# Kernel tuning notes

Hardware: AMD Instinct MI355X
Metric: run time of the kernel (lower is better)

Reference implementation:

```python
import jax, jax.numpy as jnp
import numpy as np

N_NODES = 100000
N_EDGES = 1600000
IN_F = 128
HID_F = 128
N_CLS = 40


def _linear_params(key, out_f, in_f):
    k1, k2 = jax.random.split(key)
    s = 1.0 / np.sqrt(in_f)
    w = jax.random.uniform(k1, (out_f, in_f), jnp.float32, -s, s)
    b = jax.random.uniform(k2, (out_f,), jnp.float32, -s, s)
    return w, b


def setup_inputs() -> dict:
    key = jax.random.key(0)
    ks = jax.random.split(key, 9)
    in_feat = jax.random.normal(ks[0], (N_NODES, IN_F), jnp.float32)
    src = jax.random.randint(ks[1], (N_EDGES,), 0, N_NODES, jnp.int32)
    dst = jax.random.randint(ks[2], (N_EDGES,), 0, N_NODES, jnp.int32)
    pool_w1, pool_b1 = _linear_params(ks[3], IN_F, IN_F)
    self_w1, self_b1 = _linear_params(ks[4], HID_F, IN_F)
    neigh_w1, neigh_b1 = _linear_params(ks[5], HID_F, IN_F)
    pool_w2, pool_b2 = _linear_params(ks[6], HID_F, HID_F)
    self_w2, self_b2 = _linear_params(ks[7], N_CLS, HID_F)
    neigh_w2, neigh_b2 = _linear_params(ks[8], N_CLS, HID_F)
    return dict(in_feat=in_feat, src=src, dst=dst,
                pool_w1=pool_w1, pool_b1=pool_b1, self_w1=self_w1, self_b1=self_b1,
                neigh_w1=neigh_w1, neigh_b1=neigh_b1,
                pool_w2=pool_w2, pool_b2=pool_b2, self_w2=self_w2, self_b2=self_b2,
                neigh_w2=neigh_w2, neigh_b2=neigh_b2)


def sage_conv_pool(h, src, dst, pool_w, pool_b, self_w, self_b, neigh_w, neigh_b):
    # fc_pool + relu on nodes first (N < E), then gather per edge
    m = jax.nn.relu(h @ pool_w.T + pool_b)            # [N, d]
    msgs = m[src]                                     # [E, d] gather
    agg = jax.ops.segment_max(msgs, dst, num_segments=N_NODES)  # [N, d]
    agg = jnp.where(jnp.isfinite(agg), agg, 0.0)      # zero for isolated nodes
    return h @ self_w.T + self_b + agg @ neigh_w.T + neigh_b


def reference(in_feat, src, dst,
              pool_w1, pool_b1, self_w1, self_b1, neigh_w1, neigh_b1,
              pool_w2, pool_b2, self_w2, self_b2, neigh_w2, neigh_b2):
    h = sage_conv_pool(in_feat, src, dst, pool_w1, pool_b1, self_w1, self_b1, neigh_w1, neigh_b1)
    h = jax.nn.relu(h)  # dropout is identity in eval mode
    h = sage_conv_pool(h, src, dst, pool_w2, pool_b2, self_w2, self_b2, neigh_w2, neigh_b2)
    return h
```

## Files before the change

kernel.cpp:

```cpp
#include <hip/hip_runtime.h>


#define N_FEAT 128
#define NWG_A 256
#define BSHIFT 10
#define NBMAX 128

typedef __attribute__((ext_vector_type(8))) short bf16x8;
typedef __attribute__((ext_vector_type(8))) unsigned short u16x8;
typedef __attribute__((ext_vector_type(4))) float f32x4;

static __device__ __forceinline__ unsigned short f2bf(float f) {
    unsigned u = __float_as_uint(f);
    unsigned r = (u + 0x7fffu + ((u >> 16) & 1u)) >> 16;
    return (unsigned short)r;
}

static __device__ __forceinline__ bf16x8 loadA_f32(const float* __restrict__ A, size_t idx) {
    float4 a = *(const float4*)&A[idx];
    float4 b = *(const float4*)&A[idx + 4];
    bf16x8 r;
    r[0] = (short)f2bf(a.x); r[1] = (short)f2bf(a.y);
    r[2] = (short)f2bf(a.z); r[3] = (short)f2bf(a.w);
    r[4] = (short)f2bf(b.x); r[5] = (short)f2bf(b.y);
    r[6] = (short)f2bf(b.z); r[7] = (short)f2bf(b.w);
    return r;
}

__global__ __launch_bounds__(256) void prep_bin_kernel(
    const float* __restrict__ pw1, const float* __restrict__ sw1,
    const float* __restrict__ nw1, const float* __restrict__ pw2,
    const float* __restrict__ sw2, const float* __restrict__ nw2,
    const float* __restrict__ sb1, const float* __restrict__ nb1,
    const float* __restrict__ sb2, const float* __restrict__ nb2,
    unsigned short* __restrict__ wb_p1, unsigned short* __restrict__ wb_s1,
    unsigned short* __restrict__ wb_n1, unsigned short* __restrict__ wb_p2,
    unsigned short* __restrict__ wb_s2, unsigned short* __restrict__ wb_n2,
    float* __restrict__ b_sn1, float* __restrict__ b_sn2,
    const int* __restrict__ dst, int* __restrict__ wgcnt, int E, int NB)
{
    __shared__ int cnt[NBMAX];
    if (blockIdx.x < NWG_A) {
        const int wg = blockIdx.x, tid = threadIdx.x;
        if (tid < NB) cnt[tid] = 0;
        __syncthreads();
        const int slab = (E + NWG_A - 1) / NWG_A;
        const int e0 = wg * slab;
        const int e1 = min(e0 + slab, E);
        for (int e = e0 + tid; e < e1; e += 256)
            atomicAdd(&cnt[dst[e] >> BSHIFT], 1);
        __syncthreads();
        if (tid < NB) wgcnt[tid * NWG_A + wg] = cnt[tid];
    } else {
        int t = (blockIdx.x - NWG_A) * 256 + threadIdx.x;
        if (t < 16384) {
            wb_p1[t] = f2bf(pw1[t]);
            wb_s1[t] = f2bf(sw1[t]);
            wb_n1[t] = f2bf(nw1[t]);
            wb_p2[t] = f2bf(pw2[t]);
        }
        if (t < 6144) {
            int row = t >> 7;
            wb_s2[t] = (row < 40) ? f2bf(sw2[t]) : 0;
            wb_n2[t] = (row < 40) ? f2bf(nw2[t]) : 0;
        }
        if (t < 128) b_sn1[t] = sb1[t] + nb1[t];
        if (t < 64)  b_sn2[t] = (t < 40) ? (sb2[t] + nb2[t]) : 0.f;
    }
}

__global__ __launch_bounds__(1024) void bin_scan_kernel(const int* __restrict__ wgcnt,
                                                        int* __restrict__ binoff, int NB)
{
    __shared__ int sh[1024];
    const int t = threadIdx.x;
    const int total = NB * NWG_A;
    const int chunk = (total + 1023) / 1024;
    const int b0 = t * chunk;
    const int b1 = min(b0 + chunk, total);
    int s = 0;
    for (int k = b0; k < b1; k++) s += wgcnt[k];
    sh[t] = s;
    __syncthreads();
    for (int off = 1; off < 1024; off <<= 1) {
        int x = (t >= off) ? sh[t - off] : 0;
        __syncthreads();
        sh[t] += x;
        __syncthreads();
    }
    int run = sh[t] - s;
    for (int k = b0; k < b1; k++) {
        int v = wgcnt[k];
        binoff[k] = run;
        run += v;
    }
    if (t == 1023) binoff[total] = sh[1023];
}

__global__ __launch_bounds__(256, 4) void scatter_pool_kernel(
    const int* __restrict__ src, const int* __restrict__ dst,
    const int* __restrict__ binoff, unsigned* __restrict__ binned, int E, int NB,
    const float* __restrict__ A0f, const unsigned short* __restrict__ B0,
    const float* __restrict__ bias, unsigned short* __restrict__ Cout, int M)
{
    __shared__ int cur[NBMAX];
    __shared__ unsigned short Bs[128 * 136];
    __shared__ float BsF[128];

    if (blockIdx.x < NWG_A) {
        const int wg = blockIdx.x, tid = threadIdx.x;
        if (tid < NB) cur[tid] = binoff[tid * NWG_A + wg];
        __syncthreads();
        const int slab = (E + NWG_A - 1) / NWG_A;
        const int e0 = wg * slab;
        const int e1 = min(e0 + slab, E);
        for (int e = e0 + tid; e < e1; e += 256) {
            int d = dst[e];
            int b = d >> BSHIFT;
            unsigned rec = ((unsigned)(d & ((1 << BSHIFT) - 1)) << 17) | (unsigned)src[e];
            int p = atomicAdd(&cur[b], 1);
            __builtin_nontemporal_store(rec, &binned[p]);
        }
        return;
    }

    const int tid = threadIdx.x;
    const int w = tid >> 6, lane = tid & 63;
    const int q = lane >> 4, r16 = lane & 15;
    const int m0 = (blockIdx.x - NWG_A) * 128;

    if (tid < 128) BsF[tid] = bias[tid];

    int rowA[2];
#pragma unroll
    for (int rt = 0; rt < 2; rt++) {
        int r = m0 + w * 32 + rt * 16 + r16;
        rowA[rt] = r < M ? r : (M - 1);
    }

    f32x4 acc[2][8];
#pragma unroll
    for (int i = 0; i < 2; i++)
#pragma unroll
        for (int j = 0; j < 8; j++) acc[i][j] = (f32x4){0.f, 0.f, 0.f, 0.f};

    for (int j = tid; j < 2048; j += 256) {
        int row = j >> 4, cc = j & 15;
        *(uint4*)&Bs[row * 136 + cc * 8] = *(const uint4*)&B0[(size_t)row * 128 + cc * 8];
    }
    __syncthreads();

#pragma unroll
    for (int k0 = 0; k0 < 128; k0 += 32) {
        bf16x8 af[2];
#pragma unroll
        for (int rt = 0; rt < 2; rt++)
            af[rt] = loadA_f32(A0f, (size_t)rowA[rt] * 128 + k0 + q * 8);
#pragma unroll
        for (int ct = 0; ct < 8; ct++) {
            bf16x8 bfr = *(const bf16x8*)&Bs[(ct * 16 + r16) * 136 + k0 + q * 8];
#pragma unroll
            for (int rt = 0; rt < 2; rt++)
                acc[rt][ct] = __builtin_amdgcn_mfma_f32_16x16x32_bf16(
                    af[rt], bfr, acc[rt][ct], 0, 0, 0);
        }
    }

#pragma unroll
    for (int rt = 0; rt < 2; rt++) {
#pragma unroll
        for (int ct = 0; ct < 8; ct++) {
            int col = ct * 16 + r16;
#pragma unroll
            for (int r = 0; r < 4; r++) {
                int grow = m0 + w * 32 + rt * 16 + q * 4 + r;
                if (grow < M) {
                    float v = fmaxf(acc[rt][ct][r] + BsF[col], 0.f);
                    Cout[(size_t)grow * 128 + col] = f2bf(v);
                }
            }
        }
    }
}

__global__ __launch_bounds__(1024) void csr_build_kernel(const unsigned* __restrict__ binned,
                                                         const int* __restrict__ binoff,
                                                         int* __restrict__ csr,
                                                         int* __restrict__ offsets,
                                                         int* __restrict__ counts, int M)
{
    __shared__ int cnt[1 << BSHIFT];
    __shared__ int pref[1 << BSHIFT];
    const int b = blockIdx.x, t = threadIdx.x;
    const int rs = binoff[b * NWG_A];
    const int re = binoff[(b + 1) * NWG_A];

    cnt[t] = 0;
    __syncthreads();
    for (int i = rs + t; i < re; i += 1024)
        atomicAdd(&cnt[binned[i] >> 17], 1);
    __syncthreads();

    int v = cnt[t];
    pref[t] = v;
    __syncthreads();
    for (int off = 1; off < 1024; off <<= 1) {
        int x = (t >= off) ? pref[t - off] : 0;
        __syncthreads();
        pref[t] += x;
        __syncthreads();
    }
    int excl = pref[t] - v;

    int node = (b << BSHIFT) + t;
    if (node < M) {
        counts[node] = v;
        offsets[node] = rs + excl;
    }
    cnt[t] = excl;
    __syncthreads();

    for (int i = rs + t; i < re; i += 1024) {
        unsigned r = binned[i];
        int p = atomicAdd(&cnt[r >> 17], 1);
        csr[rs + p] = (int)(r & 0x1FFFFu);
    }
}

__global__ __launch_bounds__(256) void gather_max_kernel(
    const u16x8* __restrict__ m16, const int* __restrict__ csr,
    const int* __restrict__ offsets, const int* __restrict__ counts,
    u16x8* __restrict__ agg16, int Nn)
{
    int wid = (blockIdx.x * 256 + threadIdx.x) >> 6;
    int lane = threadIdx.x & 63;
    if (wid >= Nn) return;
    const int g = lane >> 4, c = lane & 15;
    int start = offsets[wid];
    int deg = counts[wid];
    u16x8 acc = (u16x8){0, 0, 0, 0, 0, 0, 0, 0};
    for (int j0 = 0; j0 < deg; j0 += 64) {
        int nb = deg - j0;
        if (nb > 64) nb = 64;
        int sl = csr[start + j0 + (lane < nb ? lane : nb - 1)];
        for (int j = 0; j < nb; j += 4) {
            int jj = j + g;
            if (jj >= nb) jj = nb - 1;
            int s = __shfl(sl, jj);
            u16x8 v = m16[(size_t)s * 16 + c];
            acc = __builtin_elementwise_max(acc, v);
        }
    }
#pragma unroll
    for (int d = 16; d <= 32; d <<= 1) {
        int4 a = *(int4*)&acc;
        int4 t;
        t.x = __shfl_xor(a.x, d);
        t.y = __shfl_xor(a.y, d);
        t.z = __shfl_xor(a.z, d);
        t.w = __shfl_xor(a.w, d);
        acc = __builtin_elementwise_max(acc, *(u16x8*)&t);
    }
    if (g == 0) __builtin_nontemporal_store(acc, &agg16[(size_t)wid * 16 + c]);
}

template<int NT, bool RELU, int NPAIRS, bool F32OUT>
__global__ __launch_bounds__(256, 4) void mfma_gemm_kernel(
    const unsigned short* __restrict__ A0, const unsigned short* __restrict__ B0,
    const unsigned short* __restrict__ A1, const unsigned short* __restrict__ B1,
    const float* __restrict__ bias, void* __restrict__ Cout, int M, int Nout)
{
    constexpr int NR = NT * 16;
    __shared__ unsigned short Bs[NR * 136];
    __shared__ float BsF[NR];

    const int tid = threadIdx.x;
    const int w = tid >> 6, lane = tid & 63;
    const int q = lane >> 4, r16 = lane & 15;
    const int m0 = blockIdx.x * 128;

    if (tid < NR) BsF[tid] = (tid < Nout) ? bias[tid] : 0.f;

    int rowA[2];
#pragma unroll
    for (int rt = 0; rt < 2; rt++) {
        int r = m0 + w * 32 + rt * 16 + r16;
        rowA[rt] = r < M ? r : (M - 1);
    }

    f32x4 acc[2][NT];
#pragma unroll
    for (int i = 0; i < 2; i++)
#pragma unroll
        for (int j = 0; j < NT; j++) acc[i][j] = (f32x4){0.f, 0.f, 0.f, 0.f};

    for (int p = 0; p < NPAIRS; p++) {
        const unsigned short* __restrict__ B = p ? B1 : B0;
        const unsigned short* __restrict__ A = p ? A1 : A0;
        if (p) __syncthreads();
        for (int j = tid; j < NR * 16; j += 256) {
            int row = j >> 4, cc = j & 15;
            uint4 v = *(const uint4*)&B[(size_t)row * 128 + cc * 8];
            *(uint4*)&Bs[row * 136 + cc * 8] = v;
        }
        __syncthreads();

#pragma unroll
        for (int k0 = 0; k0 < 128; k0 += 32) {
            bf16x8 af[2];
#pragma unroll
            for (int rt = 0; rt < 2; rt++)
                af[rt] = *(const bf16x8*)&A[(size_t)rowA[rt] * 128 + k0 + q * 8];
#pragma unroll
            for (int ct = 0; ct < NT; ct++) {
                bf16x8 bfr = *(const bf16x8*)&Bs[(ct * 16 + r16) * 136 + k0 + q * 8];
#pragma unroll
                for (int rt = 0; rt < 2; rt++)
                    acc[rt][ct] = __builtin_amdgcn_mfma_f32_16x16x32_bf16(
                        af[rt], bfr, acc[rt][ct], 0, 0, 0);
            }
        }
    }

#pragma unroll
    for (int rt = 0; rt < 2; rt++) {
#pragma unroll
        for (int ct = 0; ct < NT; ct++) {
            int col = ct * 16 + r16;
#pragma unroll
            for (int r = 0; r < 4; r++) {
                int grow = m0 + w * 32 + rt * 16 + q * 4 + r;
                float v = acc[rt][ct][r] + BsF[col];
                if (RELU) v = fmaxf(v, 0.f);
                if (grow < M && col < Nout) {
                    if (F32OUT)
                        ((float*)Cout)[(size_t)grow * Nout + col] = v;
                    else
                        ((unsigned short*)Cout)[(size_t)grow * Nout + col] = f2bf(v);
                }
            }
        }
    }
}

__global__ __launch_bounds__(256, 2) void sn_pool_kernel(
    const float* __restrict__ A0f, const unsigned short* __restrict__ B0,
    const unsigned short* __restrict__ A1, const unsigned short* __restrict__ B1,
    const float* __restrict__ bias_sn, const unsigned short* __restrict__ Bp,
    const float* __restrict__ bias_p, unsigned short* __restrict__ h1out,
    unsigned short* __restrict__ m2out, int M)
{
    __shared__ unsigned short Bs[128 * 136];
    __shared__ unsigned short H[128 * 136];
    __shared__ float BsF[128];

    const int tid = threadIdx.x;
    const int w = tid >> 6, lane = tid & 63;
    const int q = lane >> 4, r16 = lane & 15;
    const int m0 = blockIdx.x * 128;

    if (tid < 128) BsF[tid] = bias_sn[tid];

    int rowA[2];
#pragma unroll
    for (int rt = 0; rt < 2; rt++) {
        int r = m0 + w * 32 + rt * 16 + r16;
        rowA[rt] = r < M ? r : (M - 1);
    }

    f32x4 acc[2][8];
#pragma unroll
    for (int i = 0; i < 2; i++)
#pragma unroll
        for (int j = 0; j < 8; j++) acc[i][j] = (f32x4){0.f, 0.f, 0.f, 0.f};

    for (int j = tid; j < 2048; j += 256) {
        int row = j >> 4, cc = j & 15;
        *(uint4*)&Bs[row * 136 + cc * 8] = *(const uint4*)&B0[(size_t)row * 128 + cc * 8];
    }
    __syncthreads();
#pragma unroll
    for (int k0 = 0; k0 < 128; k0 += 32) {
        bf16x8 af[2];
#pragma unroll
        for (int rt = 0; rt < 2; rt++)
            af[rt] = loadA_f32(A0f, (size_t)rowA[rt] * 128 + k0 + q * 8);
#pragma unroll
        for (int ct = 0; ct < 8; ct++) {
            bf16x8 bfr = *(const bf16x8*)&Bs[(ct * 16 + r16) * 136 + k0 + q * 8];
#pragma unroll
            for (int rt = 0; rt < 2; rt++)
                acc[rt][ct] = __builtin_amdgcn_mfma_f32_16x16x32_bf16(
                    af[rt], bfr, acc[rt][ct], 0, 0, 0);
        }
    }
    __syncthreads();

    for (int j = tid; j < 2048; j += 256) {
        int row = j >> 4, cc = j & 15;
        *(uint4*)&Bs[row * 136 + cc * 8] = *(const uint4*)&B1[(size_t)row * 128 + cc * 8];
    }
    __syncthreads();
#pragma unroll
    for (int k0 = 0; k0 < 128; k0 += 32) {
        bf16x8 af[2];
#pragma unroll
        for (int rt = 0; rt < 2; rt++)
            af[rt] = *(const bf16x8*)&A1[(size_t)rowA[rt] * 128 + k0 + q * 8];
#pragma unroll
        for (int ct = 0; ct < 8; ct++) {
            bf16x8 bfr = *(const bf16x8*)&Bs[(ct * 16 + r16) * 136 + k0 + q * 8];
#pragma unroll
            for (int rt = 0; rt < 2; rt++)
                acc[rt][ct] = __builtin_amdgcn_mfma_f32_16x16x32_bf16(
                    af[rt], bfr, acc[rt][ct], 0, 0, 0);
        }
    }

#pragma unroll
    for (int rt = 0; rt < 2; rt++) {
#pragma unroll
        for (int ct = 0; ct < 8; ct++) {
            int col = ct * 16 + r16;
#pragma unroll
            for (int r = 0; r < 4; r++) {
                int lr = w * 32 + rt * 16 + q * 4 + r;
                int grow = m0 + lr;
                float v = fmaxf(acc[rt][ct][r] + BsF[col], 0.f);
                unsigned short hb = f2bf(v);
                H[lr * 136 + col] = hb;
                if (grow < M) h1out[(size_t)grow * 128 + col] = hb;
            }
        }
    }
    __syncthreads();

    for (int j = tid; j < 2048; j += 256) {
        int row = j >> 4, cc = j & 15;
        *(uint4*)&Bs[row * 136 + cc * 8] = *(const uint4*)&Bp[(size_t)row * 128 + cc * 8];
    }
    if (tid < 128) BsF[tid] = bias_p[tid];
    __syncthreads();

#pragma unroll
    for (int i = 0; i < 2; i++)
#pragma unroll
        for (int j = 0; j < 8; j++) acc[i][j] = (f32x4){0.f, 0.f, 0.f, 0.f};

#pragma unroll
    for (int k0 = 0; k0 < 128; k0 += 32) {
        bf16x8 af[2];
#pragma unroll
        for (int rt = 0; rt < 2; rt++)
            af[rt] = *(const bf16x8*)&H[(w * 32 + rt * 16 + r16) * 136 + k0 + q * 8];
#pragma unroll
        for (int ct = 0; ct < 8; ct++) {
            bf16x8 bfr = *(const bf16x8*)&Bs[(ct * 16 + r16) * 136 + k0 + q * 8];
#pragma unroll
            for (int rt = 0; rt < 2; rt++)
                acc[rt][ct] = __builtin_amdgcn_mfma_f32_16x16x32_bf16(
                    af[rt], bfr, acc[rt][ct], 0, 0, 0);
        }
    }

#pragma unroll
    for (int rt = 0; rt < 2; rt++) {
#pragma unroll
        for (int ct = 0; ct < 8; ct++) {
            int col = ct * 16 + r16;
#pragma unroll
            for (int r = 0; r < 4; r++) {
                int grow = m0 + w * 32 + rt * 16 + q * 4 + r;
                if (grow < M) {
                    float v = fmaxf(acc[rt][ct][r] + BsF[col], 0.f);
                    m2out[(size_t)grow * 128 + col] = f2bf(v);
                }
            }
        }
    }
}

extern "C" void kernel_launch(void* const* d_in, const int* in_sizes, int n_in,
                              void* d_out, int out_size, void* d_ws, size_t ws_size,
                              hipStream_t stream)
{
    const float* in_feat = (const float*)d_in[0];
    const int*   src     = (const int*)d_in[1];
    const int*   dst     = (const int*)d_in[2];
    const float* pw1 = (const float*)d_in[3];  const float* pb1 = (const float*)d_in[4];
    const float* sw1 = (const float*)d_in[5];  const float* sb1 = (const float*)d_in[6];
    const float* nw1 = (const float*)d_in[7];  const float* nb1 = (const float*)d_in[8];
    const float* pw2 = (const float*)d_in[9];  const float* pb2 = (const float*)d_in[10];
    const float* sw2 = (const float*)d_in[11]; const float* sb2 = (const float*)d_in[12];
    const float* nw2 = (const float*)d_in[13]; const float* nb2 = (const float*)d_in[14];
    float* out = (float*)d_out;

    const int M = in_sizes[0] / N_FEAT;
    const int E = in_sizes[1];
    const int NB = (M + (1 << BSHIFT) - 1) >> BSHIFT;

    char* base = (char*)d_ws;
    size_t off = 0;
    auto alloc = [&](size_t bytes) { char* p = base + off; off = (off + bytes + 255) & ~(size_t)255; return p; };
    unsigned short* wb_p1 = (unsigned short*)alloc(16384 * 2);
    unsigned short* wb_s1 = (unsigned short*)alloc(16384 * 2);
    unsigned short* wb_n1 = (unsigned short*)alloc(16384 * 2);
    unsigned short* wb_p2 = (unsigned short*)alloc(16384 * 2);
    unsigned short* wb_s2 = (unsigned short*)alloc(6144 * 2);
    unsigned short* wb_n2 = (unsigned short*)alloc(6144 * 2);
    float* b_sn1 = (float*)alloc(128 * 4);
    float* b_sn2 = (float*)alloc(64 * 4);
    unsigned short* mb   = (unsigned short*)alloc((size_t)M * 128 * 2);
    unsigned short* agg  = (unsigned short*)alloc((size_t)M * 128 * 2);
    unsigned short* h1   = (unsigned short*)alloc((size_t)M * 128 * 2);
    int* counts  = (int*)alloc((size_t)M * 4);
    int* offsets = (int*)alloc((size_t)M * 4);
    int* wgcnt   = (int*)alloc((size_t)NB * NWG_A * 4);
    int* binoff  = (int*)alloc(((size_t)NB * NWG_A + 1) * 4);
    unsigned* binned = (unsigned*)alloc((size_t)E * 4);
    int* csr     = (int*)alloc((size_t)E * 4);

    const int gemm_grid = (M + 127) / 128;
    const int gather_grid = (M * 64 + 255) / 256;

    prep_bin_kernel<<<NWG_A + 64, 256, 0, stream>>>(
        pw1, sw1, nw1, pw2, sw2, nw2, sb1, nb1, sb2, nb2,
        wb_p1, wb_s1, wb_n1, wb_p2, wb_s2, wb_n2, b_sn1, b_sn2,
        dst, wgcnt, E, NB);
    bin_scan_kernel<<<1, 1024, 0, stream>>>(wgcnt, binoff, NB);
    scatter_pool_kernel<<<NWG_A + gemm_grid, 256, 0, stream>>>(
        src, dst, binoff, binned, E, NB,
        in_feat, wb_p1, pb1, mb, M);
    csr_build_kernel<<<NB, 1024, 0, stream>>>(binned, binoff, csr, offsets, counts, M);

    gather_max_kernel<<<gather_grid, 256, 0, stream>>>(
        (const u16x8*)mb, csr, offsets, counts, (u16x8*)agg, M);
    sn_pool_kernel<<<gemm_grid, 256, 0, stream>>>(
        in_feat, wb_s1, agg, wb_n1, b_sn1, wb_p2, pb2, h1, mb, M);

    gather_max_kernel<<<gather_grid, 256, 0, stream>>>(
        (const u16x8*)mb, csr, offsets, counts, (u16x8*)agg, M);
    mfma_gemm_kernel<3, false, 2, true><<<gemm_grid, 256, 0, stream>>>(
        h1, wb_s2, agg, wb_n2, b_sn2, out, M, 40);
}
```

Baseline: 391.6 us.

## Shrink sn_pool LDS via K-halved weight staging to allow three blocks per CU

```diff
diff --git a/kernel.cpp b/kernel.cpp
--- a/kernel.cpp
+++ b/kernel.cpp
@@ -119,7 +119,7 @@
             int b = d >> BSHIFT;
             unsigned rec = ((unsigned)(d & ((1 << BSHIFT) - 1)) << 17) | (unsigned)src[e];
             int p = atomicAdd(&cur[b], 1);
-            __builtin_nontemporal_store(rec, &binned[p]);
+            binned[p] = rec;
         }
         return;
     }
@@ -343,15 +343,15 @@
     }
 }
 
-__global__ __launch_bounds__(256, 2) void sn_pool_kernel(
+__global__ __launch_bounds__(256, 3) void sn_pool_kernel(
     const float* __restrict__ A0f, const unsigned short* __restrict__ B0,
     const unsigned short* __restrict__ A1, const unsigned short* __restrict__ B1,
     const float* __restrict__ bias_sn, const unsigned short* __restrict__ Bp,
     const float* __restrict__ bias_p, unsigned short* __restrict__ h1out,
     unsigned short* __restrict__ m2out, int M)
 {
-    __shared__ unsigned short Bs[128 * 136];
-    __shared__ unsigned short H[128 * 136];
+    __shared__ unsigned short Bs[128 * 66];
+    __shared__ unsigned short H[128 * 132];
     __shared__ float BsF[128];
 
     const int tid = threadIdx.x;
@@ -374,46 +374,37 @@
 #pragma unroll
         for (int j = 0; j < 8; j++) acc[i][j] = (f32x4){0.f, 0.f, 0.f, 0.f};
 
-    for (int j = tid; j < 2048; j += 256) {
-        int row = j >> 4, cc = j & 15;
-        *(uint4*)&Bs[row * 136 + cc * 8] = *(const uint4*)&B0[(size_t)row * 128 + cc * 8];
-    }
-    __syncthreads();
-#pragma unroll
-    for (int k0 = 0; k0 < 128; k0 += 32) {
-        bf16x8 af[2];
-#pragma unroll
-        for (int rt = 0; rt < 2; rt++)
-            af[rt] = loadA_f32(A0f, (size_t)rowA[rt] * 128 + k0 + q * 8);
-#pragma unroll
-        for (int ct = 0; ct < 8; ct++) {
-            bf16x8 bfr = *(const bf16x8*)&Bs[(ct * 16 + r16) * 136 + k0 + q * 8];
-#pragma unroll
-            for (int rt = 0; rt < 2; rt++)
-                acc[rt][ct] = __builtin_amdgcn_mfma_f32_16x16x32_bf16(
-                    af[rt], bfr, acc[rt][ct], 0, 0, 0);
-        }
-    }
-    __syncthreads();
-
-    for (int j = tid; j < 2048; j += 256) {
-        int row = j >> 4, cc = j & 15;
-        *(uint4*)&Bs[row * 136 + cc * 8] = *(const uint4*)&B1[(size_t)row * 128 + cc * 8];
-    }
-    __syncthreads();
-#pragma unroll
-    for (int k0 = 0; k0 < 128; k0 += 32) {
-        bf16x8 af[2];
-#pragma unroll
-        for (int rt = 0; rt < 2; rt++)
-            af[rt] = *(const bf16x8*)&A1[(size_t)rowA[rt] * 128 + k0 + q * 8];
-#pragma unroll
-        for (int ct = 0; ct < 8; ct++) {
-            bf16x8 bfr = *(const bf16x8*)&Bs[(ct * 16 + r16) * 136 + k0 + q * 8];
-#pragma unroll
-            for (int rt = 0; rt < 2; rt++)
-                acc[rt][ct] = __builtin_amdgcn_mfma_f32_16x16x32_bf16(
-                    af[rt], bfr, acc[rt][ct], 0, 0, 0);
+    for (int p = 0; p < 2; p++) {
+        const unsigned short* __restrict__ B = p ? B1 : B0;
+        for (int kh = 0; kh < 2; kh++) {
+            __syncthreads();
+            for (int j = tid; j < 1024; j += 256) {
+                int row = j >> 3, cc = j & 7;
+                *(uint4*)&Bs[row * 66 + cc * 8] =
+                    *(const uint4*)&B[(size_t)row * 128 + kh * 64 + cc * 8];
+            }
+            __syncthreads();
+#pragma unroll
+            for (int k0i = 0; k0i < 2; k0i++) {
+                const int k0 = kh * 64 + k0i * 32;
+                const int koff = k0i * 32;
+                bf16x8 af[2];
+#pragma unroll
+                for (int rt = 0; rt < 2; rt++) {
+                    if (p == 0)
+                        af[rt] = loadA_f32(A0f, (size_t)rowA[rt] * 128 + k0 + q * 8);
+                    else
+                        af[rt] = *(const bf16x8*)&A1[(size_t)rowA[rt] * 128 + k0 + q * 8];
+                }
+#pragma unroll
+                for (int ct = 0; ct < 8; ct++) {
+                    bf16x8 bfr = *(const bf16x8*)&Bs[(ct * 16 + r16) * 66 + koff + q * 8];
+#pragma unroll
+                    for (int rt = 0; rt < 2; rt++)
+                        acc[rt][ct] = __builtin_amdgcn_mfma_f32_16x16x32_bf16(
+                            af[rt], bfr, acc[rt][ct], 0, 0, 0);
+                }
+            }
         }
     }
 
@@ -428,38 +419,43 @@
                 int grow = m0 + lr;
                 float v = fmaxf(acc[rt][ct][r] + BsF[col], 0.f);
                 unsigned short hb = f2bf(v);
-                H[lr * 136 + col] = hb;
+                H[lr * 132 + col] = hb;
                 if (grow < M) h1out[(size_t)grow * 128 + col] = hb;
             }
         }
     }
     __syncthreads();
-
-    for (int j = tid; j < 2048; j += 256) {
-        int row = j >> 4, cc = j & 15;
-        *(uint4*)&Bs[row * 136 + cc * 8] = *(const uint4*)&Bp[(size_t)row * 128 + cc * 8];
-    }
     if (tid < 128) BsF[tid] = bias_p[tid];
-    __syncthreads();
 
 #pragma unroll
     for (int i = 0; i < 2; i++)
 #pragma unroll
         for (int j = 0; j < 8; j++) acc[i][j] = (f32x4){0.f, 0.f, 0.f, 0.f};
 
-#pragma unroll
-    for (int k0 = 0; k0 < 128; k0 += 32) {
-        bf16x8 af[2];
-#pragma unroll
-        for (int rt = 0; rt < 2; rt++)
-            af[rt] = *(const bf16x8*)&H[(w * 32 + rt * 16 + r16) * 136 + k0 + q * 8];
-#pragma unroll
-        for (int ct = 0; ct < 8; ct++) {
-            bf16x8 bfr = *(const bf16x8*)&Bs[(ct * 16 + r16) * 136 + k0 + q * 8];
+    for (int kh = 0; kh < 2; kh++) {
+        __syncthreads();
+        for (int j = tid; j < 1024; j += 256) {
+            int row = j >> 3, cc = j & 7;
+            *(uint4*)&Bs[row * 66 + cc * 8] =
+                *(const uint4*)&Bp[(size_t)row * 128 + kh * 64 + cc * 8];
+        }
+        __syncthreads();
+#pragma unroll
+        for (int k0i = 0; k0i < 2; k0i++) {
+            const int k0 = kh * 64 + k0i * 32;
+            const int koff = k0i * 32;
+            bf16x8 af[2];
 #pragma unroll
             for (int rt = 0; rt < 2; rt++)
-                acc[rt][ct] = __builtin_amdgcn_mfma_f32_16x16x32_bf16(
-                    af[rt], bfr, acc[rt][ct], 0, 0, 0);
+                af[rt] = *(const bf16x8*)&H[(w * 32 + rt * 16 + r16) * 132 + k0 + q * 8];
+#pragma unroll
+            for (int ct = 0; ct < 8; ct++) {
+                bf16x8 bfr = *(const bf16x8*)&Bs[(ct * 16 + r16) * 66 + koff + q * 8];
+#pragma unroll
+                for (int rt = 0; rt < 2; rt++)
+                    acc[rt][ct] = __builtin_amdgcn_mfma_f32_16x16x32_bf16(
+                        af[rt], bfr, acc[rt][ct], 0, 0, 0);
+            }
         }
     }
 
```

Result: faster. 376.9 us (-3.8%).
